# Kernel tuning notes

Hardware: AMD Instinct MI355X
Metric: run time of the kernel (lower is better)

Reference implementation:

```python
import jax, jax.numpy as jnp
import numpy as np

EPS = 1e-8  # numerical guard in padded (masked) softmax denominator


def setup_inputs() -> dict:
    key = jax.random.key(0)
    k1, k2 = jax.random.split(key)
    B, N, D = 8, 2048, 3
    coordinates = jax.random.normal(k1, (B, N, D), dtype=jnp.float32)
    masks = (jax.random.uniform(k2, (B, N, N)) < 0.9).astype(jnp.float32)
    sigma = jnp.ones((1,), dtype=jnp.float32)  # NonNeg learned scalar
    return {"coordinates": coordinates, "masks": masks, "sigma": sigma}


def reference(coordinates, masks, sigma):
    # pairwise squared euclidean distances: ||xi||^2 - 2 xi.xj + ||xj||^2
    norms = jnp.sum(coordinates ** 2, axis=-1, keepdims=True)            # [B,N,1]
    inner = jnp.einsum('bnd,bmd->bnm', coordinates, coordinates)         # [B,N,N]
    distances = norms - 2.0 * inner + jnp.swapaxes(norms, -1, -2)        # [B,N,N]
    # Gaussian kernel
    A = jnp.exp(-distances / (sigma ** 2))                               # [B,N,N]
    # padded_softmax: mask then row-normalize (A is positive, so this is a
    # masked softmax over -d/sigma^2 along the last axis)
    A = A * masks
    return A / (jnp.sum(A, axis=-1, keepdims=True) + EPS)
```

## Files before the change

### kernel.cpp

```cpp
#include <hip/hip_runtime.h>
#include <math.h>


#define NN 2048
#define THREADS 256
#define EPS 1e-8f

__global__ __launch_bounds__(THREADS) void gauss_adj_kernel(
    const float* __restrict__ coords,
    const float* __restrict__ masks,
    const float* __restrict__ sigma,
    float* __restrict__ out)
{
    const int row = blockIdx.x;
    const int b   = row >> 11;
    const int i   = row & (NN - 1);
    const int tid = threadIdx.x;

    __shared__ __align__(16) float sx[NN];
    __shared__ __align__(16) float sy[NN];
    __shared__ __align__(16) float sz[NN];
    __shared__ float red[THREADS / 64];
    __shared__ float s_inv;

    const float* cb = coords + (size_t)b * NN * 3;
    for (int idx = tid; idx < NN; idx += THREADS) {
        sx[idx] = cb[idx * 3 + 0];
        sy[idx] = cb[idx * 3 + 1];
        sz[idx] = cb[idx * 3 + 2];
    }
    __syncthreads();

    const float xi = sx[i];
    const float yi = sy[i];
    const float zi = sz[i];
    const float s  = sigma[0];
    const float inv_s2 = 1.0f / (s * s);

    const float4* mrow = (const float4*)(masks + (size_t)row * NN);
    float4*       orow = (float4*)(out + (size_t)row * NN);
    const float4* sx4 = (const float4*)sx;
    const float4* sy4 = (const float4*)sy;
    const float4* sz4 = (const float4*)sz;

    float vals[8];
    float lsum = 0.0f;

    #pragma unroll
    for (int c = 0; c < 2; ++c) {
        const int j4 = c * THREADS + tid;
        const float4 m = mrow[j4];
        const float4 X = sx4[j4];
        const float4 Y = sy4[j4];
        const float4 Z = sz4[j4];
        const float mx[4] = {m.x, m.y, m.z, m.w};
        const float xs[4] = {X.x, X.y, X.z, X.w};
        const float ys[4] = {Y.x, Y.y, Y.z, Y.w};
        const float zs[4] = {Z.x, Z.y, Z.z, Z.w};
        #pragma unroll
        for (int k = 0; k < 4; ++k) {
            const float dx = xi - xs[k];
            const float dy = yi - ys[k];
            const float dz = zi - zs[k];
            const float d  = dx * dx + dy * dy + dz * dz;
            const float a  = __expf(-d * inv_s2) * mx[k];
            vals[c * 4 + k] = a;
            lsum += a;
        }
    }

    #pragma unroll
    for (int off = 32; off > 0; off >>= 1)
        lsum += __shfl_down(lsum, off, 64);
    const int wave = tid >> 6;
    if ((tid & 63) == 0) red[wave] = lsum;
    __syncthreads();
    if (tid == 0) {
        float tot = red[0] + red[1] + red[2] + red[3];
        s_inv = 1.0f / (tot + EPS);
    }
    __syncthreads();
    const float inv = s_inv;

    #pragma unroll
    for (int c = 0; c < 2; ++c) {
        const int j4 = c * THREADS + tid;
        float4 o;
        o.x = vals[c * 4 + 0] * inv;
        o.y = vals[c * 4 + 1] * inv;
        o.z = vals[c * 4 + 2] * inv;
        o.w = vals[c * 4 + 3] * inv;
        orow[j4] = o;
    }
}

extern "C" void kernel_launch(void* const* d_in, const int* in_sizes, int n_in,
                              void* d_out, int out_size, void* d_ws, size_t ws_size,
                              hipStream_t stream) {
    const float* coords = (const float*)d_in[0];
    const float* masks  = (const float*)d_in[1];
    const float* sigma  = (const float*)d_in[2];
    float* out = (float*)d_out;

    const int B = in_sizes[0] / (NN * 3);
    const int rows = B * NN;
    gauss_adj_kernel<<<rows, THREADS, 0, stream>>>(coords, masks, sigma, out);
}
```

Measured before the change: 233.0 us.

## Process multiple rows per block with one wave per row and shuffle-only reduction

Each block now handles 8 rows, with each wave owning two full rows in turn, instead of one block per row. The per-batch coordinate staging into shared memory is amortized over 8 rows rather than repeated for every row. Block-level barriers and the shared-memory reduction are replaced by a wave-wide xor shuffle reduction. Each lane holds 32 values per row, which raises register pressure and reduces the number of blocks available to hide memory latency.

```diff
diff --git a/kernel.cpp b/kernel.cpp
--- a/kernel.cpp
+++ b/kernel.cpp
@@ -4,24 +4,26 @@
 
 #define NN 2048
 #define THREADS 256
+#define WAVES (THREADS / 64)
+#define ROWS_PER_WAVE 2
+#define ROWS_PER_BLOCK (WAVES * ROWS_PER_WAVE)
 #define EPS 1e-8f
 
-__global__ __launch_bounds__(THREADS) void gauss_adj_kernel(
+__global__ __launch_bounds__(THREADS, 4) void gauss_adj_kernel(
     const float* __restrict__ coords,
     const float* __restrict__ masks,
     const float* __restrict__ sigma,
     float* __restrict__ out)
 {
-    const int row = blockIdx.x;
-    const int b   = row >> 11;
-    const int i   = row & (NN - 1);
+    const int rows_base = blockIdx.x * ROWS_PER_BLOCK;
+    const int b   = rows_base >> 11;
     const int tid = threadIdx.x;
+    const int wave = tid >> 6;
+    const int lane = tid & 63;
 
     __shared__ __align__(16) float sx[NN];
     __shared__ __align__(16) float sy[NN];
     __shared__ __align__(16) float sz[NN];
-    __shared__ float red[THREADS / 64];
-    __shared__ float s_inv;
 
     const float* cb = coords + (size_t)b * NN * 3;
     for (int idx = tid; idx < NN; idx += THREADS) {
@@ -31,66 +33,68 @@
     }
     __syncthreads();
 
-    const float xi = sx[i];
-    const float yi = sy[i];
-    const float zi = sz[i];
     const float s  = sigma[0];
     const float inv_s2 = 1.0f / (s * s);
 
-    const float4* mrow = (const float4*)(masks + (size_t)row * NN);
-    float4*       orow = (float4*)(out + (size_t)row * NN);
     const float4* sx4 = (const float4*)sx;
     const float4* sy4 = (const float4*)sy;
     const float4* sz4 = (const float4*)sz;
 
-    float vals[8];
-    float lsum = 0.0f;
+    #pragma unroll
+    for (int r = 0; r < ROWS_PER_WAVE; ++r) {
+        const int row_local = wave * ROWS_PER_WAVE + r;
+        const int row = rows_base + row_local;
+        const int i   = (rows_base & (NN - 1)) + row_local;
 
-    #pragma unroll
-    for (int c = 0; c < 2; ++c) {
-        const int j4 = c * THREADS + tid;
-        const float4 m = mrow[j4];
-        const float4 X = sx4[j4];
-        const float4 Y = sy4[j4];
-        const float4 Z = sz4[j4];
-        const float mx[4] = {m.x, m.y, m.z, m.w};
-        const float xs[4] = {X.x, X.y, X.z, X.w};
-        const float ys[4] = {Y.x, Y.y, Y.z, Y.w};
-        const float zs[4] = {Z.x, Z.y, Z.z, Z.w};
+        const float xi = sx[i];
+        const float yi = sy[i];
+        const float zi = sz[i];
+
+        const float4* mrow = (const float4*)(masks + (size_t)row * NN);
+        float4*       orow = (float4*)(out + (size_t)row * NN);
+
+        float vals[32];
+        float lsum = 0.0f;
+
         #pragma unroll
-        for (int k = 0; k < 4; ++k) {
-            const float dx = xi - xs[k];
-            const float dy = yi - ys[k];
-            const float dz = zi - zs[k];
-            const float d  = dx * dx + dy * dy + dz * dz;
-            const float a  = __expf(-d * inv_s2) * mx[k];
-            vals[c * 4 + k] = a;
-            lsum += a;
+        for (int k = 0; k < 8; ++k) {
+            const int j4 = k * 64 + lane;
+            const float4 m = mrow[j4];
+            const float4 X = sx4[j4];
+            const float4 Y = sy4[j4];
+            const float4 Z = sz4[j4];
+            const float mx[4] = {m.x, m.y, m.z, m.w};
+            const float xs[4] = {X.x, X.y, X.z, X.w};
+            const float ys[4] = {Y.x, Y.y, Y.z, Y.w};
+            const float zs[4] = {Z.x, Z.y, Z.z, Z.w};
+            #pragma unroll
+            for (int q = 0; q < 4; ++q) {
+                const float dx = xi - xs[q];
+                const float dy = yi - ys[q];
+                const float dz = zi - zs[q];
+                const float d  = dx * dx + dy * dy + dz * dz;
+                const float a  = __expf(-d * inv_s2) * mx[q];
+                vals[k * 4 + q] = a;
+                lsum += a;
+            }
         }
-    }
 
-    #pragma unroll
-    for (int off = 32; off > 0; off >>= 1)
-        lsum += __shfl_down(lsum, off, 64);
-    const int wave = tid >> 6;
-    if ((tid & 63) == 0) red[wave] = lsum;
-    __syncthreads();
-    if (tid == 0) {
-        float tot = red[0] + red[1] + red[2] + red[3];
-        s_inv = 1.0f / (tot + EPS);
-    }
-    __syncthreads();
-    const float inv = s_inv;
+        #pragma unroll
+        for (int off = 1; off < 64; off <<= 1)
+            lsum += __shfl_xor(lsum, off, 64);
 
-    #pragma unroll
-    for (int c = 0; c < 2; ++c) {
-        const int j4 = c * THREADS + tid;
-        float4 o;
-        o.x = vals[c * 4 + 0] * inv;
-        o.y = vals[c * 4 + 1] * inv;
-        o.z = vals[c * 4 + 2] * inv;
-        o.w = vals[c * 4 + 3] * inv;
-        orow[j4] = o;
+        const float inv = 1.0f / (lsum + EPS);
+
+        #pragma unroll
+        for (int k = 0; k < 8; ++k) {
+            const int j4 = k * 64 + lane;
+            float4 o;
+            o.x = vals[k * 4 + 0] * inv;
+            o.y = vals[k * 4 + 1] * inv;
+            o.z = vals[k * 4 + 2] * inv;
+            o.w = vals[k * 4 + 3] * inv;
+            orow[j4] = o;
+        }
     }
 }
 
@@ -104,5 +108,5 @@
 
     const int B = in_sizes[0] / (NN * 3);
     const int rows = B * NN;
-    gauss_adj_kernel<<<rows, THREADS, 0, stream>>>(coords, masks, sigma, out);
+    gauss_adj_kernel<<<rows / ROWS_PER_BLOCK, THREADS, 0, stream>>>(coords, masks, sigma, out);
 }
```

New measurement: 329.3 us. +41.3%, slower.
